# Performance work log

Hardware: AMD Instinct MI355X
Metric: run time of the kernel (lower is better)

Reference implementation:

```python
import jax, jax.numpy as jnp
import numpy as np


def setup_inputs() -> dict:
    key = jax.random.key(0)
    k1, k2, k3 = jax.random.split(key, 3)
    B, L, D = 8, 4096, 320
    CB_DIM, N_BOOKS = 16, 8192
    input_values = jax.random.normal(k1, (B, L, D), dtype=jnp.float32)
    # mask all ones -> static masked-select shape N = B*L
    mask_time_indices = jnp.ones((B, L), dtype=jnp.int32)
    # xavier_uniform for Linear(D -> CB_DIM, bias=False): limit = sqrt(6/(fan_in+fan_out))
    limit = float(np.sqrt(6.0 / (D + CB_DIM)))
    proj_weight = jax.random.uniform(k2, (CB_DIM, D), dtype=jnp.float32, minval=-limit, maxval=limit)
    code_book = jax.random.normal(k3, (N_BOOKS, CB_DIM), dtype=jnp.float32)
    return {"input_values": input_values, "mask_time_indices": mask_time_indices,
            "proj_weight": proj_weight, "code_book": code_book}


def reference(input_values, mask_time_indices, proj_weight, code_book):
    # input_values: [B, L, D]; mask is all-ones so masked select == flatten (static shape N=B*L)
    B, L, D = input_values.shape
    flat = input_values.reshape(B * L, D)  # [N, D]
    targets = flat @ proj_weight.T  # [N, cb_dim]  (random projection, no bias)
    # argmin over Euclidean norm == argmin over squared distance (monotone),
    # expanded form avoids the [N, n_books, cb_dim] broadcast intermediate.
    t2 = jnp.sum(targets * targets, axis=-1, keepdims=True)        # [N, 1]
    c2 = jnp.sum(code_book * code_book, axis=-1)                   # [n_books]
    d2 = t2 - 2.0 * (targets @ code_book.T) + c2                   # [N, n_books]
    labels = jnp.argmin(d2, axis=-1)                               # [N]
    return labels
```

## Files before the change

### kernel.cpp

```cpp
#include <hip/hip_runtime.h>

#define N_ROWS 32768
#define D_IN 320
#define CB 16
#define N_BOOKS 8192

typedef __attribute__((ext_vector_type(8))) short bf16x8;
typedef __attribute__((ext_vector_type(4))) float f32x4;
#define MFMA __builtin_amdgcn_mfma_f32_16x16x32_bf16
#define AS1 __attribute__((address_space(1)))
#define AS3 __attribute__((address_space(3)))

__device__ __forceinline__ unsigned short bf16rn(float f) {
  unsigned u = __float_as_uint(f);
  u += 0x7fffu + ((u >> 16) & 1u);
  return (unsigned short)(u >> 16);
}
__device__ __forceinline__ float bf16tof(unsigned short h) {
  return __uint_as_float(((unsigned)h) << 16);
}
__device__ __forceinline__ void gload_lds16(const short* g, short* l) {
  __builtin_amdgcn_global_load_lds((const AS1 unsigned int*)g, (AS3 unsigned int*)l, 16, 0, 0);
}

__global__ __launch_bounds__(256, 2) void prep_proj_kernel(const float* __restrict__ cbk,
                                                           const float* __restrict__ x,
                                                           const float* __restrict__ w,
                                                           short* __restrict__ bfrag,
                                                           float* __restrict__ nh_g,
                                                           short* __restrict__ tsplit) {
  __shared__ __align__(16) short wfrag[3][10][64][8];
  __shared__ __align__(16) float xs[2][64 * 36];
  const int tid = threadIdx.x;

  if (blockIdx.x < 32) {
    const int j = blockIdx.x * 256 + tid;
    const float4* src = (const float4*)(cbk + (size_t)j * CB);
    float4 a = src[0], b = src[1], c = src[2], d = src[3];
    float ce[16] = {a.x, a.y, a.z, a.w, b.x, b.y, b.z, b.w,
                    c.x, c.y, c.z, c.w, d.x, d.y, d.z, d.w};
    short c1[16], c2[16], c3[16];
    double s = 0.0;
#pragma unroll
    for (int i = 0; i < 16; i++) {
      s += (double)ce[i] * (double)ce[i];
      unsigned short x1 = bf16rn(ce[i]);
      float r1 = ce[i] - bf16tof(x1);
      unsigned short x2 = bf16rn(r1);
      float r2 = r1 - bf16tof(x2);
      unsigned short x3 = bf16rn(r2);
      c1[i] = (short)x1; c2[i] = (short)x2; c3[i] = (short)x3;
    }
    nh_g[j] = (float)(-0.5 * s);
    bf16x8 lo1, hi1, lo2, hi2, lo3, hi3;
#pragma unroll
    for (int i = 0; i < 8; i++) {
      lo1[i] = c1[i]; hi1[i] = c1[i + 8];
      lo2[i] = c2[i]; hi2[i] = c2[i + 8];
      lo3[i] = c3[i]; hi3[i] = c3[i + 8];
    }
    short* base = bfrag + (size_t)(j >> 4) * 768;
    const int n = j & 15;
    *(bf16x8*)(base + 0 + n * 8) = lo1;
    *(bf16x8*)(base + 128 + n * 8) = hi1;
    *(bf16x8*)(base + 256 + n * 8) = lo2;
    *(bf16x8*)(base + 384 + n * 8) = hi2;
    *(bf16x8*)(base + 512 + n * 8) = lo3;
    *(bf16x8*)(base + 640 + n * 8) = hi3;
    return;
  }

  const int bid = blockIdx.x - 32;
  const int lane = tid & 63;
  const int wv = tid >> 6;

  for (int o = 0; o < CB; o++) {
    for (int dbase = 0; dbase < D_IN; dbase += 256) {
      int d = dbase + tid;
      if (d < D_IN) {
        float f = w[o * D_IN + d];
        unsigned short h1 = bf16rn(f);
        float r1 = f - bf16tof(h1);
        unsigned short h2 = bf16rn(r1);
        float r2 = r1 - bf16tof(h2);
        unsigned short h3 = bf16rn(r2);
        int c = d >> 5, qq = (d >> 3) & 3, pos = d & 7;
        int ln = qq * 16 + o;
        wfrag[0][c][ln][pos] = (short)h1;
        wfrag[1][c][ln][pos] = (short)h2;
        wfrag[2][c][ln][pos] = (short)h3;
      }
    }
  }

  const float* xblk = x + (size_t)bid * 64 * D_IN;
  {
    int row = tid >> 2, k0 = (tid & 3) * 8;
    float4 v0 = *(const float4*)(xblk + row * D_IN + k0);
    float4 v1 = *(const float4*)(xblk + row * D_IN + k0 + 4);
    *(float4*)&xs[0][row * 36 + k0] = v0;
    *(float4*)&xs[0][row * 36 + k0 + 4] = v1;
  }
  __syncthreads();

  const int m = lane & 15, q = lane >> 4;
  double dacc[4] = {0.0, 0.0, 0.0, 0.0};
  for (int c = 0; c < 10; c++) {
    const int buf = c & 1;
    if (c < 9) {
      int row = tid >> 2, k0 = (tid & 3) * 8;
      float4 v0 = *(const float4*)(xblk + row * D_IN + (c + 1) * 32 + k0);
      float4 v1 = *(const float4*)(xblk + row * D_IN + (c + 1) * 32 + k0 + 4);
      *(float4*)&xs[buf ^ 1][row * 36 + k0] = v0;
      *(float4*)&xs[buf ^ 1][row * 36 + k0 + 4] = v1;
    }
    const float* xp = &xs[buf][(wv * 16 + m) * 36 + q * 8];
    float4 xa = *(const float4*)xp;
    float4 xb = *(const float4*)(xp + 4);
    float xe[8] = {xa.x, xa.y, xa.z, xa.w, xb.x, xb.y, xb.z, xb.w};
    bf16x8 a1, a2, a3;
#pragma unroll
    for (int j = 0; j < 8; j++) {
      unsigned short h1 = bf16rn(xe[j]);
      float r1 = xe[j] - bf16tof(h1);
      unsigned short h2 = bf16rn(r1);
      float r2 = r1 - bf16tof(h2);
      unsigned short h3 = bf16rn(r2);
      a1[j] = (short)h1; a2[j] = (short)h2; a3[j] = (short)h3;
    }
    bf16x8 b1 = *(const bf16x8*)wfrag[0][c][lane];
    bf16x8 b2 = *(const bf16x8*)wfrag[1][c][lane];
    bf16x8 b3 = *(const bf16x8*)wfrag[2][c][lane];
    f32x4 g = {0.f, 0.f, 0.f, 0.f};
    g = MFMA(a1, b1, g, 0, 0, 0);
#pragma unroll
    for (int r = 0; r < 4; r++) dacc[r] += (double)g[r];
    g = (f32x4){0.f, 0.f, 0.f, 0.f};
    g = MFMA(a2, b1, g, 0, 0, 0);
    g = MFMA(a1, b2, g, 0, 0, 0);
#pragma unroll
    for (int r = 0; r < 4; r++) dacc[r] += (double)g[r];
    g = (f32x4){0.f, 0.f, 0.f, 0.f};
    g = MFMA(a3, b1, g, 0, 0, 0);
    g = MFMA(a1, b3, g, 0, 0, 0);
    g = MFMA(a2, b2, g, 0, 0, 0);
#pragma unroll
    for (int r = 0; r < 4; r++) dacc[r] += (double)g[r];
    __syncthreads();
  }

  float* tl = (float*)xs;
#pragma unroll
  for (int r = 0; r < 4; r++) tl[(wv * 16 + q * 4 + r) * 17 + m] = (float)dacc[r];
  __syncthreads();
  {
    int row_l = tid >> 2, p = tid & 3;
    short h1[4], h2[4], h3[4];
#pragma unroll
    for (int i = 0; i < 4; i++) {
      float f = tl[row_l * 17 + p * 4 + i];
      unsigned short a = bf16rn(f);
      float r1 = f - bf16tof(a);
      unsigned short b = bf16rn(r1);
      float r2 = r1 - bf16tof(b);
      unsigned short cc = bf16rn(r2);
      h1[i] = (short)a; h2[i] = (short)b; h3[i] = (short)cc;
    }
    size_t base = (size_t)(bid * 64 + row_l) * 48;
    *(short4*)(tsplit + base + p * 4) = make_short4(h1[0], h1[1], h1[2], h1[3]);
    *(short4*)(tsplit + base + 16 + p * 4) = make_short4(h2[0], h2[1], h2[2], h2[3]);
    *(short4*)(tsplit + base + 32 + p * 4) = make_short4(h3[0], h3[1], h3[2], h3[3]);
  }
}

#define SC_H 8

__global__ __launch_bounds__(256, 4) void score_kernel(const short* __restrict__ tsplit,
                                                       const short* __restrict__ bfrag,
                                                       const float* __restrict__ nh_g,
                                                       float* __restrict__ cs1,
                                                       float* __restrict__ cs2,
                                                       int* __restrict__ cidx) {
  __shared__ __align__(16) short ldsb[2][6144];
  __shared__ float ldsnh[1024];
  const int tid = threadIdx.x;
  const int lane = tid & 63;
  const int wv = tid >> 6;
  const int m = lane & 15, q = lane >> 4;
  const int rb = blockIdx.x & 127;
  const int h = blockIdx.x >> 7;
  const int rowbase = rb * 256;

  bf16x8 A12[4], A13[4];
#pragma unroll
  for (int rt = 0; rt < 4; rt++) {
    int row = rowbase + wv * 64 + rt * 16 + m;
    const short* tp = tsplit + (size_t)row * 48;
    A12[rt] = *(const bf16x8*)(tp + q * 8);
    A13[rt] = *(const bf16x8*)(tp + q * 8 + ((q >= 2) ? 16 : 0));
  }
  for (int i = tid; i < 1024; i += 256) ldsnh[i] = nh_g[h * 1024 + i];

  const short* gq = bfrag + (size_t)h * 49152;
  {
    const short* g0 = gq + wv * 1536 + lane * 8;
#pragma unroll
    for (int it = 0; it < 3; it++)
      gload_lds16(g0 + it * 512, &ldsb[0][wv * 1536 + it * 512]);
  }

  float s1[4][4], s2[4][4];
  int i1[4][4];
#pragma unroll
  for (int rt = 0; rt < 4; rt++)
#pragma unroll
    for (int r = 0; r < 4; r++) { s1[rt][r] = -3.4e38f; s2[rt][r] = -3.4e38f; i1[rt][r] = 0; }

  __syncthreads();

  for (int sc = 0; sc < 8; sc++) {
    const int cur = sc & 1;
    if (sc < 7) {
      const short* gs = gq + (sc + 1) * 6144 + wv * 1536 + lane * 8;
#pragma unroll
      for (int it = 0; it < 3; it++)
        gload_lds16(gs + it * 512, &ldsb[cur ^ 1][wv * 1536 + it * 512]);
    }
#pragma unroll 2
    for (int bt = 0; bt < 8; bt++) {
      const short* bp = &ldsb[cur][bt * 768];
      const int l31 = (lane & 31) * 8;
      bf16x8 b1 = *(const bf16x8*)(bp + l31);
      bf16x8 b2 = *(const bf16x8*)(bp + 256 + l31);
      bf16x8 b3 = *(const bf16x8*)(bp + ((lane < 32) ? 512 : 0) + l31);
      const int btg = sc * 8 + bt;
      float nh0 = ldsnh[btg * 16 + m];
      f32x4 ci = {nh0, nh0, nh0, nh0};
      const int colv = h * 1024 + btg * 16 + m;
#pragma unroll
      for (int rt = 0; rt < 4; rt++) {
        f32x4 acc = MFMA(A12[rt], b1, ci, 0, 0, 0);
        acc = MFMA(A12[rt], b2, acc, 0, 0, 0);
        acc = MFMA(A13[rt], b3, acc, 0, 0, 0);
#pragma unroll
        for (int r = 0; r < 4; r++) {
          float v = acc[r];
          float s1o = s1[rt][r];
          s2[rt][r] = __builtin_amdgcn_fmed3f(v, s1o, s2[rt][r]);
          s1[rt][r] = fmaxf(s1o, v);
          i1[rt][r] = (v > s1o) ? colv : i1[rt][r];
        }
      }
    }
    __syncthreads();
  }

#pragma unroll
  for (int rt = 0; rt < 4; rt++)
#pragma unroll
    for (int r = 0; r < 4; r++) {
      float a1v = s1[rt][r], a2v = s2[rt][r];
      int ai = i1[rt][r];
#pragma unroll
      for (int msk = 1; msk <= 8; msk <<= 1) {
        float o1 = __shfl_xor(a1v, msk);
        float o2 = __shfl_xor(a2v, msk);
        int oi = __shfl_xor(ai, msk);
        if (o1 > a1v) {
          a2v = fmaxf(a1v, o2); a1v = o1; ai = oi;
        } else {
          a2v = fmaxf(a2v, o1);
          if (o1 == a1v && oi < ai) ai = oi;
        }
      }
      if (m == 0) {
        int row = rowbase + wv * 64 + rt * 16 + q * 4 + r;
        size_t idx = (size_t)h * N_ROWS + row;
        cs1[idx] = a1v; cs2[idx] = a2v; cidx[idx] = ai;
      }
    }
}

#define MARGIN_EPS 1.0e-4f

__global__ __launch_bounds__(256) void reduce_fb_kernel(const float* __restrict__ cs1,
                                                        const float* __restrict__ cs2,
                                                        const int* __restrict__ cidx,
                                                        const float* __restrict__ x,
                                                        const float* __restrict__ w,
                                                        const float* __restrict__ codebook,
                                                        int* __restrict__ out) {
  __shared__ int flagged[256];
  __shared__ double ps[16][17];
  __shared__ double tsh[16];
  __shared__ double rs[256];
  __shared__ int ri[256];
  const int tid = threadIdx.x;
  const int base = blockIdx.x * 256;
  {
    const int r = base + tid;
    float S1 = -3.4e38f, S2 = -3.4e38f;
    int I = 0;
#pragma unroll
    for (int h = 0; h < SC_H; h++) {
      size_t idx = (size_t)h * N_ROWS + r;
      float v1 = cs1[idx], v2 = cs2[idx];
      if (v1 > S1) {
        S2 = fmaxf(S1, v2); S1 = v1; I = cidx[idx];
      } else {
        S2 = fmaxf(S2, v1);
      }
    }
    out[r] = I;
    flagged[tid] = (S1 - S2 < MARGIN_EPS) ? 1 : 0;
  }
  __syncthreads();

  for (int rr = 0; rr < 256; rr++) {
    if (!flagged[rr]) continue;
    const int row = base + rr;
    {
      int o = tid & 15, c = tid >> 4;
      double p = 0.0;
      for (int k = 0; k < 20; k++) {
        int d = c * 20 + k;
        p = fma((double)x[(size_t)row * D_IN + d], (double)w[o * D_IN + d], p);
      }
      ps[c][o] = p;
    }
    __syncthreads();
    if (tid < 16) {
      double t = 0.0;
      for (int c = 0; c < 16; c++) t += ps[c][tid];
      tsh[tid] = t;
    }
    __syncthreads();
    double t[16];
#pragma unroll
    for (int i = 0; i < 16; i++) t[i] = tsh[i];
    double bs = -1.0e300;
    int bi = 0;
    for (int j = tid; j < N_BOOKS; j += 256) {
      const float* cp = codebook + (size_t)j * CB;
      double dot = 0.0, cc = 0.0;
#pragma unroll
      for (int i = 0; i < 16; i++) {
        double cv = (double)cp[i];
        dot = fma(t[i], cv, dot);
        cc = fma(cv, cv, cc);
      }
      double mv = dot - 0.5 * cc;
      if (mv > bs) { bs = mv; bi = j; }
    }
    rs[tid] = bs; ri[tid] = bi;
    __syncthreads();
    for (int s = 128; s > 0; s >>= 1) {
      if (tid < s) {
        double os = rs[tid + s]; int oi = ri[tid + s];
        if (os > rs[tid] || (os == rs[tid] && oi < ri[tid])) { rs[tid] = os; ri[tid] = oi; }
      }
      __syncthreads();
    }
    if (tid == 0) out[row] = ri[0];
    __syncthreads();
  }
}

extern "C" void kernel_launch(void* const* d_in, const int* in_sizes, int n_in,
                              void* d_out, int out_size, void* d_ws, size_t ws_size,
                              hipStream_t stream) {
  (void)in_sizes; (void)n_in; (void)out_size; (void)ws_size;
  const float* x = (const float*)d_in[0];
  const float* w = (const float*)d_in[2];
  const float* codebook = (const float*)d_in[3];

  char* ws = (char*)d_ws;
  short* tsplit = (short*)(ws);
  short* bfrag = (short*)(ws + 3145728);
  float* nh_g = (float*)(ws + 3932160);
  float* cs1 = (float*)(ws + (4 << 20));
  float* cs2 = (float*)(ws + (5 << 20));
  int* cidx = (int*)(ws + (6 << 20));
  int* out = (int*)d_out;

  prep_proj_kernel<<<32 + N_ROWS / 64, 256, 0, stream>>>(codebook, x, w, bfrag, nh_g, tsplit);
  score_kernel<<<128 * SC_H, 256, 0, stream>>>(tsplit, bfrag, nh_g, cs1, cs2, cidx);
  reduce_fb_kernel<<<N_ROWS / 256, 256, 0, stream>>>(cs1, cs2, cidx, x, w, codebook, out);
}
```

Before: 208.6 us.

## Use two-term bf16 split with error-bounded margin and compacted fallback list

Drops the third bf16 term of the codebook and target splits, so each score tile needs two MFMAs instead of three and the fragment buffers are smaller. To keep exact results it tracks the global max squared norms of targets and codes and uses them to set a margin that bounds the bf16 truncation error. Rows whose top-two gap falls inside that margin are appended atomically to a list and recomputed in double by a separate grid-strided fallback kernel. The score kernel now splits the codebook into 16 chunks with smaller LDS buffers and higher occupancy. In exchange, the wider margin may flag more rows for the slow fallback, and there are extra atomics, a memset and one more kernel launch.

```diff
diff --git a/kernel.cpp b/kernel.cpp
--- a/kernel.cpp
+++ b/kernel.cpp
@@ -22,15 +22,21 @@
 __device__ __forceinline__ void gload_lds16(const short* g, short* l) {
   __builtin_amdgcn_global_load_lds((const AS1 unsigned int*)g, (AS3 unsigned int*)l, 16, 0, 0);
 }
+__device__ __forceinline__ void atomicMaxPosF(int* addr, float v) {
+  atomicMax(addr, __float_as_int(v));
+}
 
 __global__ __launch_bounds__(256, 2) void prep_proj_kernel(const float* __restrict__ cbk,
                                                            const float* __restrict__ x,
                                                            const float* __restrict__ w,
                                                            short* __restrict__ bfrag,
                                                            float* __restrict__ nh_g,
-                                                           short* __restrict__ tsplit) {
+                                                           short* __restrict__ tsplit,
+                                                           int* __restrict__ gmaxT2,
+                                                           int* __restrict__ gmaxC2) {
   __shared__ __align__(16) short wfrag[3][10][64][8];
   __shared__ __align__(16) float xs[2][64 * 36];
+  __shared__ float wred[4];
   const int tid = threadIdx.x;
 
   if (blockIdx.x < 32) {
@@ -39,7 +45,7 @@
     float4 a = src[0], b = src[1], c = src[2], d = src[3];
     float ce[16] = {a.x, a.y, a.z, a.w, b.x, b.y, b.z, b.w,
                     c.x, c.y, c.z, c.w, d.x, d.y, d.z, d.w};
-    short c1[16], c2[16], c3[16];
+    short c1[16], c2[16];
     double s = 0.0;
 #pragma unroll
     for (int i = 0; i < 16; i++) {
@@ -47,26 +53,28 @@
       unsigned short x1 = bf16rn(ce[i]);
       float r1 = ce[i] - bf16tof(x1);
       unsigned short x2 = bf16rn(r1);
-      float r2 = r1 - bf16tof(x2);
-      unsigned short x3 = bf16rn(r2);
-      c1[i] = (short)x1; c2[i] = (short)x2; c3[i] = (short)x3;
+      c1[i] = (short)x1; c2[i] = (short)x2;
     }
     nh_g[j] = (float)(-0.5 * s);
-    bf16x8 lo1, hi1, lo2, hi2, lo3, hi3;
+    bf16x8 lo1, hi1, lo2, hi2;
 #pragma unroll
     for (int i = 0; i < 8; i++) {
       lo1[i] = c1[i]; hi1[i] = c1[i + 8];
       lo2[i] = c2[i]; hi2[i] = c2[i + 8];
-      lo3[i] = c3[i]; hi3[i] = c3[i + 8];
-    }
-    short* base = bfrag + (size_t)(j >> 4) * 768;
+    }
+    short* base = bfrag + (size_t)(j >> 4) * 512;
     const int n = j & 15;
     *(bf16x8*)(base + 0 + n * 8) = lo1;
     *(bf16x8*)(base + 128 + n * 8) = hi1;
     *(bf16x8*)(base + 256 + n * 8) = lo2;
     *(bf16x8*)(base + 384 + n * 8) = hi2;
-    *(bf16x8*)(base + 512 + n * 8) = lo3;
-    *(bf16x8*)(base + 640 + n * 8) = hi3;
+    float c2f = (float)s;
+#pragma unroll
+    for (int msk = 1; msk <= 32; msk <<= 1) c2f = fmaxf(c2f, __shfl_xor(c2f, msk));
+    if ((tid & 63) == 0) wred[tid >> 6] = c2f;
+    __syncthreads();
+    if (tid == 0)
+      atomicMaxPosF(gmaxC2, fmaxf(fmaxf(wred[0], wred[1]), fmaxf(wred[2], wred[3])));
     return;
   }
 
@@ -155,59 +163,59 @@
   __syncthreads();
   {
     int row_l = tid >> 2, p = tid & 3;
-    short h1[4], h2[4], h3[4];
+    short h1[4], h2[4];
+    float ss = 0.f;
 #pragma unroll
     for (int i = 0; i < 4; i++) {
       float f = tl[row_l * 17 + p * 4 + i];
+      ss = fmaf(f, f, ss);
       unsigned short a = bf16rn(f);
       float r1 = f - bf16tof(a);
       unsigned short b = bf16rn(r1);
-      float r2 = r1 - bf16tof(b);
-      unsigned short cc = bf16rn(r2);
-      h1[i] = (short)a; h2[i] = (short)b; h3[i] = (short)cc;
-    }
-    size_t base = (size_t)(bid * 64 + row_l) * 48;
+      h1[i] = (short)a; h2[i] = (short)b;
+    }
+    size_t base = (size_t)(bid * 64 + row_l) * 32;
     *(short4*)(tsplit + base + p * 4) = make_short4(h1[0], h1[1], h1[2], h1[3]);
     *(short4*)(tsplit + base + 16 + p * 4) = make_short4(h2[0], h2[1], h2[2], h2[3]);
-    *(short4*)(tsplit + base + 32 + p * 4) = make_short4(h3[0], h3[1], h3[2], h3[3]);
-  }
-}
-
-#define SC_H 8
-
-__global__ __launch_bounds__(256, 4) void score_kernel(const short* __restrict__ tsplit,
+    ss += __shfl_xor(ss, 1);
+    ss += __shfl_xor(ss, 2);
+#pragma unroll
+    for (int msk = 4; msk <= 32; msk <<= 1) ss = fmaxf(ss, __shfl_xor(ss, msk));
+    if (lane == 0) wred[wv] = ss;
+  }
+  __syncthreads();
+  if (tid == 0)
+    atomicMaxPosF(gmaxT2, fmaxf(fmaxf(wred[0], wred[1]), fmaxf(wred[2], wred[3])));
+}
+
+#define SC_NCH 16
+
+__global__ __launch_bounds__(256, 5) void score_kernel(const short* __restrict__ tsplit,
                                                        const short* __restrict__ bfrag,
                                                        const float* __restrict__ nh_g,
                                                        float* __restrict__ cs1,
                                                        float* __restrict__ cs2,
                                                        int* __restrict__ cidx) {
-  __shared__ __align__(16) short ldsb[2][6144];
-  __shared__ float ldsnh[1024];
+  __shared__ __align__(16) short ldsb[2][2048];
+  __shared__ float ldsnh[512];
   const int tid = threadIdx.x;
   const int lane = tid & 63;
   const int wv = tid >> 6;
   const int m = lane & 15, q = lane >> 4;
   const int rb = blockIdx.x & 127;
-  const int h = blockIdx.x >> 7;
+  const int ch = blockIdx.x >> 7;
   const int rowbase = rb * 256;
 
-  bf16x8 A12[4], A13[4];
+  bf16x8 A12[4];
 #pragma unroll
   for (int rt = 0; rt < 4; rt++) {
     int row = rowbase + wv * 64 + rt * 16 + m;
-    const short* tp = tsplit + (size_t)row * 48;
-    A12[rt] = *(const bf16x8*)(tp + q * 8);
-    A13[rt] = *(const bf16x8*)(tp + q * 8 + ((q >= 2) ? 16 : 0));
-  }
-  for (int i = tid; i < 1024; i += 256) ldsnh[i] = nh_g[h * 1024 + i];
-
-  const short* gq = bfrag + (size_t)h * 49152;
-  {
-    const short* g0 = gq + wv * 1536 + lane * 8;
-#pragma unroll
-    for (int it = 0; it < 3; it++)
-      gload_lds16(g0 + it * 512, &ldsb[0][wv * 1536 + it * 512]);
-  }
+    A12[rt] = *(const bf16x8*)(tsplit + (size_t)row * 32 + (q & 1) * 8 + ((q >= 2) ? 16 : 0));
+  }
+  for (int i = tid; i < 512; i += 256) ldsnh[i] = nh_g[ch * 512 + i];
+
+  const short* gq = bfrag + (size_t)ch * 16384;
+  gload_lds16(gq + wv * 512 + lane * 8, &ldsb[0][wv * 512]);
 
   float s1[4][4], s2[4][4];
   int i1[4][4];
@@ -220,28 +228,22 @@
 
   for (int sc = 0; sc < 8; sc++) {
     const int cur = sc & 1;
-    if (sc < 7) {
-      const short* gs = gq + (sc + 1) * 6144 + wv * 1536 + lane * 8;
-#pragma unroll
-      for (int it = 0; it < 3; it++)
-        gload_lds16(gs + it * 512, &ldsb[cur ^ 1][wv * 1536 + it * 512]);
-    }
-#pragma unroll 2
-    for (int bt = 0; bt < 8; bt++) {
-      const short* bp = &ldsb[cur][bt * 768];
+    if (sc < 7)
+      gload_lds16(gq + (sc + 1) * 2048 + wv * 512 + lane * 8, &ldsb[cur ^ 1][wv * 512]);
+#pragma unroll
+    for (int bt = 0; bt < 4; bt++) {
+      const short* bp = &ldsb[cur][bt * 512];
       const int l31 = (lane & 31) * 8;
       bf16x8 b1 = *(const bf16x8*)(bp + l31);
       bf16x8 b2 = *(const bf16x8*)(bp + 256 + l31);
-      bf16x8 b3 = *(const bf16x8*)(bp + ((lane < 32) ? 512 : 0) + l31);
-      const int btg = sc * 8 + bt;
+      const int btg = sc * 4 + bt;
       float nh0 = ldsnh[btg * 16 + m];
       f32x4 ci = {nh0, nh0, nh0, nh0};
-      const int colv = h * 1024 + btg * 16 + m;
+      const int colv = ch * 512 + btg * 16 + m;
 #pragma unroll
       for (int rt = 0; rt < 4; rt++) {
         f32x4 acc = MFMA(A12[rt], b1, ci, 0, 0, 0);
         acc = MFMA(A12[rt], b2, acc, 0, 0, 0);
-        acc = MFMA(A13[rt], b3, acc, 0, 0, 0);
 #pragma unroll
         for (int r = 0; r < 4; r++) {
           float v = acc[r];
@@ -275,50 +277,56 @@
       }
       if (m == 0) {
         int row = rowbase + wv * 64 + rt * 16 + q * 4 + r;
-        size_t idx = (size_t)h * N_ROWS + row;
+        size_t idx = (size_t)ch * N_ROWS + row;
         cs1[idx] = a1v; cs2[idx] = a2v; cidx[idx] = ai;
       }
     }
 }
 
-#define MARGIN_EPS 1.0e-4f
-
-__global__ __launch_bounds__(256) void reduce_fb_kernel(const float* __restrict__ cs1,
-                                                        const float* __restrict__ cs2,
-                                                        const int* __restrict__ cidx,
-                                                        const float* __restrict__ x,
-                                                        const float* __restrict__ w,
-                                                        const float* __restrict__ codebook,
-                                                        int* __restrict__ out) {
-  __shared__ int flagged[256];
+__global__ __launch_bounds__(256) void reduce_kernel(const float* __restrict__ cs1,
+                                                     const float* __restrict__ cs2,
+                                                     const int* __restrict__ cidx,
+                                                     const int* __restrict__ gmaxT2,
+                                                     const int* __restrict__ gmaxC2,
+                                                     int* __restrict__ out,
+                                                     int* __restrict__ list,
+                                                     int* __restrict__ nflag) {
+  const int r = blockIdx.x * 256 + threadIdx.x;
+  const float margin =
+      1.220703125e-4f * sqrtf(__int_as_float(*gmaxT2) * __int_as_float(*gmaxC2)) + 1.0e-4f;
+  float S1 = -3.4e38f, S2 = -3.4e38f;
+  int I = 0;
+#pragma unroll
+  for (int ch = 0; ch < SC_NCH; ch++) {
+    size_t idx = (size_t)ch * N_ROWS + r;
+    float v1 = cs1[idx], v2 = cs2[idx];
+    if (v1 > S1) {
+      S2 = fmaxf(S1, v2); S1 = v1; I = cidx[idx];
+    } else {
+      S2 = fmaxf(S2, v1);
+    }
+  }
+  out[r] = I;
+  if (S1 - S2 < margin) {
+    int slot = atomicAdd(nflag, 1);
+    list[slot] = r;
+  }
+}
+
+__global__ __launch_bounds__(256) void fb_kernel(const int* __restrict__ list,
+                                                 const int* __restrict__ nflag,
+                                                 const float* __restrict__ x,
+                                                 const float* __restrict__ w,
+                                                 const float* __restrict__ codebook,
+                                                 int* __restrict__ out) {
   __shared__ double ps[16][17];
   __shared__ double tsh[16];
   __shared__ double rs[256];
   __shared__ int ri[256];
   const int tid = threadIdx.x;
-  const int base = blockIdx.x * 256;
-  {
-    const int r = base + tid;
-    float S1 = -3.4e38f, S2 = -3.4e38f;
-    int I = 0;
-#pragma unroll
-    for (int h = 0; h < SC_H; h++) {
-      size_t idx = (size_t)h * N_ROWS + r;
-      float v1 = cs1[idx], v2 = cs2[idx];
-      if (v1 > S1) {
-        S2 = fmaxf(S1, v2); S1 = v1; I = cidx[idx];
-      } else {
-        S2 = fmaxf(S2, v1);
-      }
-    }
-    out[r] = I;
-    flagged[tid] = (S1 - S2 < MARGIN_EPS) ? 1 : 0;
-  }
-  __syncthreads();
-
-  for (int rr = 0; rr < 256; rr++) {
-    if (!flagged[rr]) continue;
-    const int row = base + rr;
+  const int cnt = *nflag;
+  for (int i = blockIdx.x; i < cnt; i += gridDim.x) {
+    const int row = list[i];
     {
       int o = tid & 15, c = tid >> 4;
       double p = 0.0;
@@ -337,16 +345,16 @@
     __syncthreads();
     double t[16];
 #pragma unroll
-    for (int i = 0; i < 16; i++) t[i] = tsh[i];
+    for (int k = 0; k < 16; k++) t[k] = tsh[k];
     double bs = -1.0e300;
     int bi = 0;
     for (int j = tid; j < N_BOOKS; j += 256) {
       const float* cp = codebook + (size_t)j * CB;
       double dot = 0.0, cc = 0.0;
 #pragma unroll
-      for (int i = 0; i < 16; i++) {
-        double cv = (double)cp[i];
-        dot = fma(t[i], cv, dot);
+      for (int k = 0; k < 16; k++) {
+        double cv = (double)cp[k];
+        dot = fma(t[k], cv, dot);
         cc = fma(cv, cv, cc);
       }
       double mv = dot - 0.5 * cc;
@@ -376,14 +384,22 @@
 
   char* ws = (char*)d_ws;
   short* tsplit = (short*)(ws);
-  short* bfrag = (short*)(ws + 3145728);
-  float* nh_g = (float*)(ws + 3932160);
-  float* cs1 = (float*)(ws + (4 << 20));
+  short* bfrag = (short*)(ws + (2 << 20));
+  float* nh_g = (float*)(ws + 2621440);
+  float* cs1 = (float*)(ws + (3 << 20));
   float* cs2 = (float*)(ws + (5 << 20));
-  int* cidx = (int*)(ws + (6 << 20));
+  int* cidx = (int*)(ws + (7 << 20));
+  int* list = (int*)(ws + (9 << 20));
+  int* scalars = (int*)(ws + (9 << 20) + (128 << 10));
+  int* nflag = scalars;
+  int* gmaxT2 = scalars + 1;
+  int* gmaxC2 = scalars + 2;
   int* out = (int*)d_out;
 
-  prep_proj_kernel<<<32 + N_ROWS / 64, 256, 0, stream>>>(codebook, x, w, bfrag, nh_g, tsplit);
-  score_kernel<<<128 * SC_H, 256, 0, stream>>>(tsplit, bfrag, nh_g, cs1, cs2, cidx);
-  reduce_fb_kernel<<<N_ROWS / 256, 256, 0, stream>>>(cs1, cs2, cidx, x, w, codebook, out);
-}
+  hipMemsetAsync(scalars, 0, 3 * sizeof(int), stream);
+  prep_proj_kernel<<<32 + N_ROWS / 64, 256, 0, stream>>>(codebook, x, w, bfrag, nh_g, tsplit,
+                                                         gmaxT2, gmaxC2);
+  score_kernel<<<128 * SC_NCH, 256, 0, stream>>>(tsplit, bfrag, nh_g, cs1, cs2, cidx);
+  reduce_kernel<<<N_ROWS / 256, 256, 0, stream>>>(cs1, cs2, cidx, gmaxT2, gmaxC2, out, list, nflag);
+  fb_kernel<<<64, 256, 0, stream>>>(list, nflag, x, w, codebook, out);
+}
```

Result: slower. 315.0 us (+51.0%).
